# Kernel tuning notes

Measured on AMD Instinct MI355X. Metric: run time of the kernel, lower is better.

The kernel has to match this reference:

```python
import jax, jax.numpy as jnp
import numpy as np
import math

H = 16
D_MODEL = 1024
D_K = D_MODEL // H
B = 4
S = 2048


def setup_inputs() -> dict:
    key = jax.random.key(0)
    ks = jax.random.split(key, 11)
    s_in = 1.0 / math.sqrt(D_MODEL)
    inp = {
        "query": jax.random.normal(ks[0], (B, S, D_MODEL), dtype=jnp.float32),
        "key_": jax.random.normal(ks[1], (B, S, D_MODEL), dtype=jnp.float32),
        "value": jax.random.normal(ks[2], (B, S, D_MODEL), dtype=jnp.float32),
        # stacked per-head projection weights: [h, d_model, d_k]
        "Wq": jax.random.uniform(ks[3], (H, D_MODEL, D_K), jnp.float32, -s_in, s_in),
        "bq": jax.random.uniform(ks[4], (H, D_K), jnp.float32, -s_in, s_in),
        "Wk": jax.random.uniform(ks[5], (H, D_MODEL, D_K), jnp.float32, -s_in, s_in),
        "bk": jax.random.uniform(ks[6], (H, D_K), jnp.float32, -s_in, s_in),
        "Wv": jax.random.uniform(ks[7], (H, D_MODEL, D_K), jnp.float32, -s_in, s_in),
        "bv": jax.random.uniform(ks[8], (H, D_K), jnp.float32, -s_in, s_in),
        "Wo": jax.random.uniform(ks[9], (D_MODEL, D_MODEL), jnp.float32, -s_in, s_in),
        "bo": jax.random.uniform(ks[10], (D_MODEL,), jnp.float32, -s_in, s_in),
    }
    return inp


def reference(query, key_, value, Wq, bq, Wk, bk, Wv, bv, Wo, bo):
    # Per-head projections, batched over heads: [b,s,m] x [h,m,k] -> [b,h,s,k]
    q = jnp.einsum("bsm,hmk->bhsk", query, Wq) + bq[None, :, None, :]
    k = jnp.einsum("bsm,hmk->bhsk", key_, Wk) + bk[None, :, None, :]
    v = jnp.einsum("bsm,hmk->bhsk", value, Wv) + bv[None, :, None, :]
    # scores: q @ k^T -> [b,h,Sq,Sk]
    scores = jnp.einsum("bhqk,bhsk->bhqs", q, k) / jnp.sqrt(jnp.float32(D_K))
    # NOTE: original code softmaxes over dim=1 of the per-head [N,Sq,Sk]
    # tensor, i.e. the QUERY axis (axis=2 here). Mask has no effect
    # (masked_fill result is discarded in the source), so it is omitted.
    attn = jax.nn.softmax(scores, axis=2)
    ctx = jnp.einsum("bhqs,bhsk->bhqk", attn, v)  # [b,h,Sq,d_k]
    # concat heads along last dim (head-major order matches torch.cat)
    ctx = jnp.transpose(ctx, (0, 2, 1, 3)).reshape(B, S, D_MODEL)
    out = ctx @ Wo.T + bo  # final_W; dropout = identity (eval mode)
    return out
```

## Files before the change

### kernel.cpp

```cpp
#include <hip/hip_runtime.h>


#define DEV __device__ __forceinline__

typedef __bf16 bf16x8 __attribute__((ext_vector_type(8)));
typedef float  f32x4  __attribute__((ext_vector_type(4)));

DEV unsigned short f2bf(float f) {
    __bf16 h = (__bf16)f;
    return __builtin_bit_cast(unsigned short, h);
}

DEV bf16x8 ldfrag(const unsigned short* p) {
    return *reinterpret_cast<const bf16x8*>(p);
}

DEV float fast_exp2(float x) {
#if __has_builtin(__builtin_amdgcn_exp2f)
    return __builtin_amdgcn_exp2f(x);
#else
    return exp2f(x);
#endif
}

DEV void gld16(const unsigned short* g, unsigned short* l) {
    __builtin_amdgcn_global_load_lds(
        (__attribute__((address_space(1))) void*)g,
        (__attribute__((address_space(3))) void*)l, 16, 0, 0);
}

#define MFMA(a,b,c) __builtin_amdgcn_mfma_f32_16x16x32_bf16((a),(b),(c),0,0,0)

#define QSCALE 0.18033688011112042f

__global__ __launch_bounds__(256) void wprep(const float* __restrict__ Wq,
                                             const float* __restrict__ Wk,
                                             const float* __restrict__ Wv,
                                             const float* __restrict__ Wo,
                                             unsigned short* __restrict__ Wt,
                                             unsigned short* __restrict__ Wot) {
    int idx = blockIdx.x * 256 + threadIdx.x;
    int which = blockIdx.y;
    if (which == 3) { Wot[idx] = f2bf(Wo[idx]); return; }
    const float* W = (which == 0) ? Wq : (which == 1) ? Wk : Wv;
    int n = idx >> 10, m = idx & 1023;
    int h = n >> 6, k = n & 63;
    Wt[(size_t)which * 1048576 + idx] = f2bf(W[h * 65536 + m * 64 + k]);
}

__global__ __launch_bounds__(256) void xprep(const float* __restrict__ X,
                                             unsigned short* __restrict__ Xb) {
    int idx = (blockIdx.x * 256 + threadIdx.x) * 4;
    float4 f = *(const float4*)&X[idx];
    ushort4 o;
    o.x = f2bf(f.x); o.y = f2bf(f.y); o.z = f2bf(f.z); o.w = f2bf(f.w);
    *(ushort4*)&Xb[idx] = o;
}

__global__ __launch_bounds__(256) void proj_gemm(
        const unsigned short* __restrict__ Xb, const unsigned short* __restrict__ Bt,
        const float* __restrict__ bias, unsigned short* __restrict__ O,
        unsigned short* __restrict__ Vt, int z) {
    const int tid = threadIdx.x;
    const int bm = blockIdx.x, bn = blockIdx.y;

    __shared__ __align__(16) unsigned short As[128 * 32];
    __shared__ __align__(16) unsigned short Bs[128 * 32];

    const int lane = tid & 63, wid = tid >> 6;
    const int l16 = lane & 15, quad = lane >> 4;
    const int wm = wid & 1, wn = wid >> 1;

    const unsigned short* ga =
        Xb + (size_t)(bm * 128 + wid * 32 + (lane >> 2)) * 1024 + (lane & 3) * 8;
    const unsigned short* gb =
        Bt + (size_t)(bn * 128 + wid * 32 + (lane >> 2)) * 1024 + (lane & 3) * 8;
    unsigned short* la = &As[wid * 32 * 32];
    unsigned short* lb = &Bs[wid * 32 * 32];

    f32x4 acc[4][4] = {};
    for (int kt = 0; kt < 32; ++kt) {
        __syncthreads();
        const int k0 = kt * 32;
        gld16(ga + k0, la);
        gld16(ga + k0 + 16 * 1024, la + 16 * 32);
        gld16(gb + k0, lb);
        gld16(gb + k0 + 16 * 1024, lb + 16 * 32);
        __syncthreads();
        bf16x8 af[4], bfr[4];
#pragma unroll
        for (int mi = 0; mi < 4; ++mi)
            af[mi] = ldfrag(&As[(wm * 64 + mi * 16 + l16) * 32 + quad * 8]);
#pragma unroll
        for (int ni = 0; ni < 4; ++ni)
            bfr[ni] = ldfrag(&Bs[(wn * 64 + ni * 16 + l16) * 32 + quad * 8]);
#pragma unroll
        for (int mi = 0; mi < 4; ++mi)
#pragma unroll
            for (int ni = 0; ni < 4; ++ni)
                acc[mi][ni] = MFMA(af[mi], bfr[ni], acc[mi][ni]);
    }

#pragma unroll
    for (int mi = 0; mi < 4; ++mi)
#pragma unroll
        for (int ni = 0; ni < 4; ++ni)
#pragma unroll
            for (int r = 0; r < 4; ++r) {
                int row = bm * 128 + wm * 64 + mi * 16 + quad * 4 + r;
                int col = bn * 128 + wn * 64 + ni * 16 + l16;
                float v = acc[mi][ni][r] + bias[col];
                if (z == 0) v *= QSCALE;
                int b = row >> 11, s = row & 2047;
                int h = col >> 6, k = col & 63;
                unsigned short o = f2bf(v);
                if (z == 2) {
                    Vt[(size_t)((b * 16 + h) * 64 + k) * 2048 + s] = o;
                } else {
                    O[(size_t)((b * 16 + h) * 2048 + s) * 64 + k] = o;
                }
            }
}

__global__ __launch_bounds__(256) void colsum_vscale(
        const unsigned short* __restrict__ Qh, const unsigned short* __restrict__ Kh,
        unsigned short* __restrict__ Vt) {
    const int tid = threadIdx.x;
    const int st = blockIdx.x, bh = blockIdx.y;
    const unsigned short* Qb = Qh + (size_t)bh * 2048 * 64;
    const unsigned short* Kb = Kh + (size_t)bh * 2048 * 64;

    __shared__ __align__(16) unsigned short Qs[2][2][128 * 32];
    __shared__ float Dtmp[2][128];
    __shared__ float Dsh[128];

    const int lane = tid & 63, wid = tid >> 6;
    const int l16 = lane & 15, quad = lane >> 4;
    const int wm = wid & 1, wn = wid >> 1;

    bf16x8 kf[2][4];
#pragma unroll
    for (int ks = 0; ks < 2; ++ks)
#pragma unroll
        for (int ni = 0; ni < 4; ++ni)
            kf[ks][ni] = ldfrag(&Kb[(size_t)(st * 128 + wn * 64 + ni * 16 + l16) * 64 +
                                    ks * 32 + quad * 8]);

    const unsigned short* gq =
        Qb + (size_t)(wid * 32 + (lane >> 2)) * 64 + (lane & 3) * 8;

#pragma unroll
    for (int ks = 0; ks < 2; ++ks) {
        gld16(gq + ks * 32, &Qs[0][ks][wid * 32 * 32]);
        gld16(gq + (size_t)16 * 64 + ks * 32, &Qs[0][ks][(wid * 32 + 16) * 32]);
    }

    float psum[4] = {0.f, 0.f, 0.f, 0.f};
    for (int it = 0; it < 16; ++it) {
        const int buf = it & 1;
        __syncthreads();
        if (it < 15) {
            const size_t q1 = (size_t)(it + 1) * 128;
#pragma unroll
            for (int ks = 0; ks < 2; ++ks) {
                gld16(gq + q1 * 64 + ks * 32, &Qs[buf ^ 1][ks][wid * 32 * 32]);
                gld16(gq + (q1 + 16) * 64 + ks * 32,
                      &Qs[buf ^ 1][ks][(wid * 32 + 16) * 32]);
            }
        }
        f32x4 acc[4][4] = {};
#pragma unroll
        for (int ks = 0; ks < 2; ++ks) {
            bf16x8 af[4];
#pragma unroll
            for (int mi = 0; mi < 4; ++mi)
                af[mi] = ldfrag(&Qs[buf][ks][(wm * 64 + mi * 16 + l16) * 32 + quad * 8]);
#pragma unroll
            for (int mi = 0; mi < 4; ++mi)
#pragma unroll
                for (int ni = 0; ni < 4; ++ni)
                    acc[mi][ni] = MFMA(af[mi], kf[ks][ni], acc[mi][ni]);
        }
#pragma unroll
        for (int ni = 0; ni < 4; ++ni) {
            float d = 0.f;
#pragma unroll
            for (int mi = 0; mi < 4; ++mi)
#pragma unroll
                for (int r = 0; r < 4; ++r)
                    d += fast_exp2(acc[mi][ni][r]);
            psum[ni] += d;
        }
    }
#pragma unroll
    for (int ni = 0; ni < 4; ++ni) {
        float v = psum[ni];
        v += __shfl_xor(v, 16, 64);
        v += __shfl_xor(v, 32, 64);
        if (quad == 0) Dtmp[wm][wn * 64 + ni * 16 + l16] = v;
    }
    __syncthreads();
    if (tid < 128) Dsh[tid] = 1.0f / (Dtmp[0][tid] + Dtmp[1][tid]);
    __syncthreads();

    const int k = tid >> 2, c = tid & 3;
    unsigned short* vrow = Vt + ((size_t)bh * 64 + k) * 2048 + st * 128 + c * 32;
#pragma unroll
    for (int j = 0; j < 4; ++j) {
        bf16x8 v = *(const bf16x8*)&vrow[j * 8];
        bf16x8 o;
#pragma unroll
        for (int e = 0; e < 8; ++e)
            o[e] = (__bf16)((float)v[e] * Dsh[c * 32 + j * 8 + e]);
        *(bf16x8*)&vrow[j * 8] = o;
    }
}

__global__ __launch_bounds__(256) void attnpv(const unsigned short* __restrict__ Qh,
                                              const unsigned short* __restrict__ Kh,
                                              const unsigned short* __restrict__ Vn,
                                              unsigned short* __restrict__ Ctx) {
    const int tid = threadIdx.x;
    const int qt = blockIdx.x, bh = blockIdx.y;
    const int b = bh >> 4, h = bh & 15;
    const unsigned short* Qb = Qh + (size_t)bh * 2048 * 64;
    const unsigned short* Kb = Kh + (size_t)bh * 2048 * 64;
    const unsigned short* Vb = Vn + (size_t)bh * 64 * 2048;

    __shared__ __align__(16) unsigned short Ks[2][2][64 * 32];
    __shared__ __align__(16) unsigned short Vs[2][2][64 * 32];
    __shared__ __align__(16) unsigned short Ps[128 * 72];

    const int lane = tid & 63, wid = tid >> 6;
    const int l16 = lane & 15, quad = lane >> 4;
    const int wq = wid & 1, ws = wid >> 1;
    const int swz = (l16 & 3) << 3;

    bf16x8 qf[2][4];
#pragma unroll
    for (int ks = 0; ks < 2; ++ks)
#pragma unroll
        for (int nj = 0; nj < 4; ++nj)
            qf[ks][nj] = ldfrag(&Qb[(size_t)(qt * 128 + wq * 64 + nj * 16 + l16) * 64 +
                                    ks * 32 + quad * 8]);

    const int srow = lane >> 2, scol = (lane & 3) * 8, half = wid & 1;
    const unsigned short* gk = Kb + (size_t)srow * 64 + half * 32 + scol;
    const unsigned short* gv = Vb + (size_t)srow * 2048 + half * 32 + scol;

    if (wid < 2) {
#pragma unroll
        for (int gi = 0; gi < 4; ++gi)
            gld16(gk + (size_t)gi * 16 * 64, &Ks[0][half][gi * 16 * 32]);
    } else {
#pragma unroll
        for (int gi = 0; gi < 4; ++gi)
            gld16(gv + (size_t)gi * 16 * 2048, &Vs[0][half][gi * 16 * 32]);
    }

    f32x4 cacc[2][4] = {};
    for (int it = 0; it < 32; ++it) {
        const int buf = it & 1;
        const int s0 = it * 64;
        __syncthreads();

        bf16x8 kf[2][2];
#pragma unroll
        for (int mi = 0; mi < 2; ++mi)
#pragma unroll
            for (int ks = 0; ks < 2; ++ks)
                kf[mi][ks] = ldfrag(&Ks[buf][ks][(ws * 32 + mi * 16 + l16) * 32 + quad * 8]);
        f32x4 sacc[2][4] = {};
#pragma unroll
        for (int ks = 0; ks < 2; ++ks)
#pragma unroll
            for (int mi = 0; mi < 2; ++mi)
#pragma unroll
                for (int nj = 0; nj < 4; ++nj)
                    sacc[mi][nj] = MFMA(kf[mi][ks], qf[ks][nj], sacc[mi][nj]);

#pragma unroll
        for (int mi = 0; mi < 2; ++mi)
#pragma unroll
            for (int nj = 0; nj < 4; ++nj) {
                ushort4 p;
                p.x = f2bf(fast_exp2(sacc[mi][nj][0]));
                p.y = f2bf(fast_exp2(sacc[mi][nj][1]));
                p.z = f2bf(fast_exp2(sacc[mi][nj][2]));
                p.w = f2bf(fast_exp2(sacc[mi][nj][3]));
                *(ushort4*)&Ps[(size_t)(wq * 64 + nj * 16 + l16) * 72 +
                               ((ws * 32 + mi * 16 + quad * 4) ^ swz)] = p;
            }
        __syncthreads();

        if (it < 31) {
            if (wid < 2) {
#pragma unroll
                for (int gi = 0; gi < 4; ++gi)
                    gld16(gk + (size_t)(s0 + 64 + gi * 16) * 64,
                          &Ks[buf ^ 1][half][gi * 16 * 32]);
            } else {
#pragma unroll
                for (int gi = 0; gi < 4; ++gi)
                    gld16(gv + (size_t)(gi * 16) * 2048 + s0 + 64,
                          &Vs[buf ^ 1][half][gi * 16 * 32]);
            }
        }

        bf16x8 vf[2][2], pf[2][4];
#pragma unroll
        for (int mi = 0; mi < 2; ++mi)
#pragma unroll
            for (int ks2 = 0; ks2 < 2; ++ks2)
                vf[mi][ks2] = ldfrag(&Vs[buf][ks2][(ws * 32 + mi * 16 + l16) * 32 + quad * 8]);
#pragma unroll
        for (int ks2 = 0; ks2 < 2; ++ks2)
#pragma unroll
            for (int nj = 0; nj < 4; ++nj)
                pf[ks2][nj] = ldfrag(&Ps[(size_t)(wq * 64 + nj * 16 + l16) * 72 +
                                         ((ks2 * 32 + quad * 8) ^ swz)]);
#pragma unroll
        for (int ks2 = 0; ks2 < 2; ++ks2)
#pragma unroll
            for (int mi = 0; mi < 2; ++mi)
#pragma unroll
                for (int nj = 0; nj < 4; ++nj)
                    cacc[mi][nj] = MFMA(vf[mi][ks2], pf[ks2][nj], cacc[mi][nj]);
    }

#pragma unroll
    for (int mi = 0; mi < 2; ++mi)
#pragma unroll
        for (int nj = 0; nj < 4; ++nj) {
            int q = qt * 128 + wq * 64 + nj * 16 + l16;
            int k = ws * 32 + mi * 16 + quad * 4;
            ushort4 o;
            o.x = f2bf(cacc[mi][nj][0]);
            o.y = f2bf(cacc[mi][nj][1]);
            o.z = f2bf(cacc[mi][nj][2]);
            o.w = f2bf(cacc[mi][nj][3]);
            *(ushort4*)&Ctx[(size_t)(b * 2048 + q) * 1024 + h * 64 + k] = o;
        }
}

__global__ __launch_bounds__(256) void out_gemm(const unsigned short* __restrict__ A,
                                                const unsigned short* __restrict__ Bt,
                                                const float* __restrict__ bias,
                                                float* __restrict__ Out) {
    const int tid = threadIdx.x;
    const int bm = blockIdx.x, bn = blockIdx.y;

    __shared__ __align__(16) unsigned short As[128 * 32];
    __shared__ __align__(16) unsigned short Bs[128 * 32];

    const int lane = tid & 63, wid = tid >> 6;
    const int l16 = lane & 15, quad = lane >> 4;
    const int wm = wid & 1, wn = wid >> 1;

    const unsigned short* ga =
        A + (size_t)(bm * 128 + wid * 32 + (lane >> 2)) * 1024 + (lane & 3) * 8;
    const unsigned short* gb =
        Bt + (size_t)(bn * 128 + wid * 32 + (lane >> 2)) * 1024 + (lane & 3) * 8;
    unsigned short* la = &As[wid * 32 * 32];
    unsigned short* lb = &Bs[wid * 32 * 32];

    f32x4 acc[4][4] = {};
    for (int kt = 0; kt < 32; ++kt) {
        __syncthreads();
        const int k0 = kt * 32;
        gld16(ga + k0, la);
        gld16(ga + k0 + 16 * 1024, la + 16 * 32);
        gld16(gb + k0, lb);
        gld16(gb + k0 + 16 * 1024, lb + 16 * 32);
        __syncthreads();
        bf16x8 af[4], bfr[4];
#pragma unroll
        for (int mi = 0; mi < 4; ++mi)
            af[mi] = ldfrag(&As[(wm * 64 + mi * 16 + l16) * 32 + quad * 8]);
#pragma unroll
        for (int ni = 0; ni < 4; ++ni)
            bfr[ni] = ldfrag(&Bs[(wn * 64 + ni * 16 + l16) * 32 + quad * 8]);
#pragma unroll
        for (int mi = 0; mi < 4; ++mi)
#pragma unroll
            for (int ni = 0; ni < 4; ++ni)
                acc[mi][ni] = MFMA(af[mi], bfr[ni], acc[mi][ni]);
    }
#pragma unroll
    for (int mi = 0; mi < 4; ++mi)
#pragma unroll
        for (int ni = 0; ni < 4; ++ni)
#pragma unroll
            for (int r = 0; r < 4; ++r) {
                int row = bm * 128 + wm * 64 + mi * 16 + quad * 4 + r;
                int col = bn * 128 + wn * 64 + ni * 16 + l16;
                Out[(size_t)row * 1024 + col] = acc[mi][ni][r] + bias[col];
            }
}

extern "C" void kernel_launch(void* const* d_in, const int* in_sizes, int n_in,
                              void* d_out, int out_size, void* d_ws, size_t ws_size,
                              hipStream_t stream) {
    (void)in_sizes; (void)n_in; (void)out_size; (void)ws_size;
    const float* X[3] = {(const float*)d_in[0], (const float*)d_in[1],
                         (const float*)d_in[2]};
    const float* Wq = (const float*)d_in[3];
    const float* bq = (const float*)d_in[4];
    const float* Wk = (const float*)d_in[5];
    const float* bk = (const float*)d_in[6];
    const float* Wv = (const float*)d_in[7];
    const float* bv = (const float*)d_in[8];
    const float* Wo = (const float*)d_in[9];
    const float* bo = (const float*)d_in[10];
    const float* bias[3] = {bq, bk, bv};
    float* Out = (float*)d_out;

    char* ws = (char*)d_ws;
    const size_t MB = 1024 * 1024;
    unsigned short* Wt  = (unsigned short*)(ws);
    unsigned short* Wot = (unsigned short*)(ws + 6 * MB);
    unsigned short* Qh  = (unsigned short*)(ws + 8 * MB);
    unsigned short* Kh  = (unsigned short*)(ws + 24 * MB);
    unsigned short* Vt  = (unsigned short*)(ws + 40 * MB);
    unsigned short* Ctx = (unsigned short*)(ws + 56 * MB);
    unsigned short* Xb  = Ctx;
    unsigned short* Oz[3] = {Qh, Kh, Qh };

    wprep<<<dim3(4096, 4), dim3(256), 0, stream>>>(Wq, Wk, Wv, Wo, Wt, Wot);
    for (int z = 0; z < 3; ++z) {
        xprep<<<dim3(8192), dim3(256), 0, stream>>>(X[z], Xb);
        proj_gemm<<<dim3(64, 8), dim3(256), 0, stream>>>(
            Xb, Wt + (size_t)z * 1048576, bias[z], Oz[z], Vt, z);
    }
    colsum_vscale<<<dim3(16, 64), dim3(256), 0, stream>>>(Qh, Kh, Vt);
    attnpv<<<dim3(16, 64), dim3(256), 0, stream>>>(Qh, Kh, Vt, Ctx);
    out_gemm<<<dim3(64, 8), dim3(256), 0, stream>>>(Ctx, Wot, bo, Out);
}
```

Before: 456.6 us.

## Software-pipeline attention loop: overlap previous PV MFMA with current QK and exp

Restructures the attention main loop so the P·V product for the previous tile runs in the same iteration as the QK^T scores and exp of the current tile. The P buffer is double-buffered and V loads are moved to the start of each iteration. This drops one __syncthreads per iteration and lets exp/VALU work interleave with MFMA. In exchange, LDS use grows from about 34KB to about 52KB per block, which may lower occupancy, and an epilogue is added to finish the last PV step.

```diff
diff --git a/kernel.cpp b/kernel.cpp
--- a/kernel.cpp
+++ b/kernel.cpp
@@ -229,7 +229,7 @@
 
     __shared__ __align__(16) unsigned short Ks[2][2][64 * 32];
     __shared__ __align__(16) unsigned short Vs[2][2][64 * 32];
-    __shared__ __align__(16) unsigned short Ps[128 * 72];
+    __shared__ __align__(16) unsigned short Ps[2][128 * 72];
 
     const int lane = tid & 63, wid = tid >> 6;
     const int l16 = lane & 15, quad = lane >> 4;
@@ -252,24 +252,33 @@
 #pragma unroll
         for (int gi = 0; gi < 4; ++gi)
             gld16(gk + (size_t)gi * 16 * 64, &Ks[0][half][gi * 16 * 32]);
-    } else {
-#pragma unroll
-        for (int gi = 0; gi < 4; ++gi)
-            gld16(gv + (size_t)gi * 16 * 2048, &Vs[0][half][gi * 16 * 32]);
     }
 
     f32x4 cacc[2][4] = {};
     for (int it = 0; it < 32; ++it) {
-        const int buf = it & 1;
-        const int s0 = it * 64;
-        __syncthreads();
+        const int pb = it & 1;
+        __syncthreads();
+
+        if (wid < 2) {
+            if (it < 31) {
+                const size_t s1 = (size_t)(it + 1) * 64;
+#pragma unroll
+                for (int gi = 0; gi < 4; ++gi)
+                    gld16(gk + (s1 + gi * 16) * 64, &Ks[pb ^ 1][half][gi * 16 * 32]);
+            }
+        } else {
+#pragma unroll
+            for (int gi = 0; gi < 4; ++gi)
+                gld16(gv + (size_t)(gi * 16) * 2048 + it * 64,
+                      &Vs[pb][half][gi * 16 * 32]);
+        }
 
         bf16x8 kf[2][2];
 #pragma unroll
         for (int mi = 0; mi < 2; ++mi)
 #pragma unroll
             for (int ks = 0; ks < 2; ++ks)
-                kf[mi][ks] = ldfrag(&Ks[buf][ks][(ws * 32 + mi * 16 + l16) * 32 + quad * 8]);
+                kf[mi][ks] = ldfrag(&Ks[pb][ks][(ws * 32 + mi * 16 + l16) * 32 + quad * 8]);
         f32x4 sacc[2][4] = {};
 #pragma unroll
         for (int ks = 0; ks < 2; ++ks)
@@ -278,6 +287,22 @@
 #pragma unroll
                 for (int nj = 0; nj < 4; ++nj)
                     sacc[mi][nj] = MFMA(kf[mi][ks], qf[ks][nj], sacc[mi][nj]);
+
+        bf16x8 vf[2][2], pf2[2][4];
+        if (it > 0) {
+#pragma unroll
+            for (int mi = 0; mi < 2; ++mi)
+#pragma unroll
+                for (int ks2 = 0; ks2 < 2; ++ks2)
+                    vf[mi][ks2] =
+                        ldfrag(&Vs[pb ^ 1][ks2][(ws * 32 + mi * 16 + l16) * 32 + quad * 8]);
+#pragma unroll
+            for (int ks2 = 0; ks2 < 2; ++ks2)
+#pragma unroll
+                for (int nj = 0; nj < 4; ++nj)
+                    pf2[ks2][nj] = ldfrag(&Ps[pb ^ 1][(size_t)(wq * 64 + nj * 16 + l16) * 72 +
+                                              ((ks2 * 32 + quad * 8) ^ swz)]);
+        }
 
 #pragma unroll
         for (int mi = 0; mi < 2; ++mi)
@@ -288,44 +313,42 @@
                 p.y = f2bf(fast_exp2(sacc[mi][nj][1]));
                 p.z = f2bf(fast_exp2(sacc[mi][nj][2]));
                 p.w = f2bf(fast_exp2(sacc[mi][nj][3]));
-                *(ushort4*)&Ps[(size_t)(wq * 64 + nj * 16 + l16) * 72 +
-                               ((ws * 32 + mi * 16 + quad * 4) ^ swz)] = p;
+                *(ushort4*)&Ps[pb][(size_t)(wq * 64 + nj * 16 + l16) * 72 +
+                                   ((ws * 32 + mi * 16 + quad * 4) ^ swz)] = p;
             }
-        __syncthreads();
-
-        if (it < 31) {
-            if (wid < 2) {
-#pragma unroll
-                for (int gi = 0; gi < 4; ++gi)
-                    gld16(gk + (size_t)(s0 + 64 + gi * 16) * 64,
-                          &Ks[buf ^ 1][half][gi * 16 * 32]);
-            } else {
-#pragma unroll
-                for (int gi = 0; gi < 4; ++gi)
-                    gld16(gv + (size_t)(gi * 16) * 2048 + s0 + 64,
-                          &Vs[buf ^ 1][half][gi * 16 * 32]);
-            }
-        }
-
-        bf16x8 vf[2][2], pf[2][4];
+
+        if (it > 0) {
+#pragma unroll
+            for (int ks2 = 0; ks2 < 2; ++ks2)
+#pragma unroll
+                for (int mi = 0; mi < 2; ++mi)
+#pragma unroll
+                    for (int nj = 0; nj < 4; ++nj)
+                        cacc[mi][nj] = MFMA(vf[mi][ks2], pf2[ks2][nj], cacc[mi][nj]);
+        }
+    }
+
+    __syncthreads();
+    {
+        bf16x8 vf[2][2], pf2[2][4];
 #pragma unroll
         for (int mi = 0; mi < 2; ++mi)
 #pragma unroll
             for (int ks2 = 0; ks2 < 2; ++ks2)
-                vf[mi][ks2] = ldfrag(&Vs[buf][ks2][(ws * 32 + mi * 16 + l16) * 32 + quad * 8]);
+                vf[mi][ks2] = ldfrag(&Vs[1][ks2][(ws * 32 + mi * 16 + l16) * 32 + quad * 8]);
 #pragma unroll
         for (int ks2 = 0; ks2 < 2; ++ks2)
 #pragma unroll
             for (int nj = 0; nj < 4; ++nj)
-                pf[ks2][nj] = ldfrag(&Ps[(size_t)(wq * 64 + nj * 16 + l16) * 72 +
-                                         ((ks2 * 32 + quad * 8) ^ swz)]);
+                pf2[ks2][nj] = ldfrag(&Ps[1][(size_t)(wq * 64 + nj * 16 + l16) * 72 +
+                                          ((ks2 * 32 + quad * 8) ^ swz)]);
 #pragma unroll
         for (int ks2 = 0; ks2 < 2; ++ks2)
 #pragma unroll
             for (int mi = 0; mi < 2; ++mi)
 #pragma unroll
                 for (int nj = 0; nj < 4; ++nj)
-                    cacc[mi][nj] = MFMA(vf[mi][ks2], pf[ks2][nj], cacc[mi][nj]);
+                    cacc[mi][nj] = MFMA(vf[mi][ks2], pf2[ks2][nj], cacc[mi][nj]);
     }
 
 #pragma unroll
```

After: 454.1 us. About the same (-0.5%).

## Split PV over key halves per warp to drop mid-iteration block barrier

Applied to the files above, without the earlier changes.

Each warp now keeps its own private P tile in shared memory and does the PV product over only the key slice it computed, holding all 64 output columns. Because no warp reads another warp's P, the second __syncthreads per iteration goes away, and the K/V prefetch for the next tile is issued at the top of the loop. The cost is a doubled context accumulator (more registers) and a final cross-warp reduction through shared memory before the output is written.

```diff
diff --git a/kernel.cpp b/kernel.cpp
--- a/kernel.cpp
+++ b/kernel.cpp
@@ -227,14 +227,15 @@
     const unsigned short* Kb = Kh + (size_t)bh * 2048 * 64;
     const unsigned short* Vb = Vn + (size_t)bh * 64 * 2048;
 
-    __shared__ __align__(16) unsigned short Ks[2][2][64 * 32];
-    __shared__ __align__(16) unsigned short Vs[2][2][64 * 32];
-    __shared__ __align__(16) unsigned short Ps[128 * 72];
+    __shared__ __align__(16) unsigned char smem[49152];
+    unsigned short* Ks = (unsigned short*)smem;
+    unsigned short* Vs = (unsigned short*)(smem + 16384);
+    unsigned short* Pw = (unsigned short*)(smem + 32768) + (tid >> 6) * 2048;
 
     const int lane = tid & 63, wid = tid >> 6;
     const int l16 = lane & 15, quad = lane >> 4;
     const int wq = wid & 1, ws = wid >> 1;
-    const int swz = (l16 & 3) << 3;
+    const int pq = l16 & 3;
 
     bf16x8 qf[2][4];
 #pragma unroll
@@ -251,25 +252,40 @@
     if (wid < 2) {
 #pragma unroll
         for (int gi = 0; gi < 4; ++gi)
-            gld16(gk + (size_t)gi * 16 * 64, &Ks[0][half][gi * 16 * 32]);
+            gld16(gk + (size_t)gi * 16 * 64, &Ks[half * 2048 + gi * 16 * 32]);
     } else {
 #pragma unroll
         for (int gi = 0; gi < 4; ++gi)
-            gld16(gv + (size_t)gi * 16 * 2048, &Vs[0][half][gi * 16 * 32]);
-    }
-
-    f32x4 cacc[2][4] = {};
+            gld16(gv + (size_t)gi * 16 * 2048, &Vs[half * 2048 + gi * 16 * 32]);
+    }
+
+    f32x4 cacc[4][4] = {};
     for (int it = 0; it < 32; ++it) {
-        const int buf = it & 1;
-        const int s0 = it * 64;
-        __syncthreads();
+        const int pb = it & 1;
+        __syncthreads();
+
+        if (it < 31) {
+            const size_t s1 = (size_t)(it + 1) * 64;
+            if (wid < 2) {
+#pragma unroll
+                for (int gi = 0; gi < 4; ++gi)
+                    gld16(gk + (s1 + gi * 16) * 64,
+                          &Ks[((pb ^ 1) * 2 + half) * 2048 + gi * 16 * 32]);
+            } else {
+#pragma unroll
+                for (int gi = 0; gi < 4; ++gi)
+                    gld16(gv + (size_t)(gi * 16) * 2048 + s1,
+                          &Vs[((pb ^ 1) * 2 + half) * 2048 + gi * 16 * 32]);
+            }
+        }
 
         bf16x8 kf[2][2];
 #pragma unroll
         for (int mi = 0; mi < 2; ++mi)
 #pragma unroll
             for (int ks = 0; ks < 2; ++ks)
-                kf[mi][ks] = ldfrag(&Ks[buf][ks][(ws * 32 + mi * 16 + l16) * 32 + quad * 8]);
+                kf[mi][ks] = ldfrag(&Ks[(pb * 2 + ks) * 2048 +
+                                        (ws * 32 + mi * 16 + l16) * 32 + quad * 8]);
         f32x4 sacc[2][4] = {};
 #pragma unroll
         for (int ks = 0; ks < 2; ++ks)
@@ -280,7 +296,8 @@
                     sacc[mi][nj] = MFMA(kf[mi][ks], qf[ks][nj], sacc[mi][nj]);
 
 #pragma unroll
-        for (int mi = 0; mi < 2; ++mi)
+        for (int mi = 0; mi < 2; ++mi) {
+            const int gsw = ((mi * 2 + (quad >> 1)) ^ pq) * 8 + (quad & 1) * 4;
 #pragma unroll
             for (int nj = 0; nj < 4; ++nj) {
                 ushort4 p;
@@ -288,59 +305,50 @@
                 p.y = f2bf(fast_exp2(sacc[mi][nj][1]));
                 p.z = f2bf(fast_exp2(sacc[mi][nj][2]));
                 p.w = f2bf(fast_exp2(sacc[mi][nj][3]));
-                *(ushort4*)&Ps[(size_t)(wq * 64 + nj * 16 + l16) * 72 +
-                               ((ws * 32 + mi * 16 + quad * 4) ^ swz)] = p;
-            }
-        __syncthreads();
-
-        if (it < 31) {
-            if (wid < 2) {
-#pragma unroll
-                for (int gi = 0; gi < 4; ++gi)
-                    gld16(gk + (size_t)(s0 + 64 + gi * 16) * 64,
-                          &Ks[buf ^ 1][half][gi * 16 * 32]);
-            } else {
-#pragma unroll
-                for (int gi = 0; gi < 4; ++gi)
-                    gld16(gv + (size_t)(gi * 16) * 2048 + s0 + 64,
-                          &Vs[buf ^ 1][half][gi * 16 * 32]);
+                *(ushort4*)&Pw[(nj * 16 + l16) * 32 + gsw] = p;
             }
         }
 
-        bf16x8 vf[2][2], pf[2][4];
-#pragma unroll
-        for (int mi = 0; mi < 2; ++mi)
-#pragma unroll
-            for (int ks2 = 0; ks2 < 2; ++ks2)
-                vf[mi][ks2] = ldfrag(&Vs[buf][ks2][(ws * 32 + mi * 16 + l16) * 32 + quad * 8]);
-#pragma unroll
-        for (int ks2 = 0; ks2 < 2; ++ks2)
+        bf16x8 vf[4], pf[4];
+#pragma unroll
+        for (int mi = 0; mi < 4; ++mi)
+            vf[mi] = ldfrag(&Vs[(pb * 2 + ws) * 2048 + (mi * 16 + l16) * 32 + quad * 8]);
+#pragma unroll
+        for (int nj = 0; nj < 4; ++nj)
+            pf[nj] = ldfrag(&Pw[(nj * 16 + l16) * 32 + (quad ^ pq) * 8]);
+#pragma unroll
+        for (int mi = 0; mi < 4; ++mi)
 #pragma unroll
             for (int nj = 0; nj < 4; ++nj)
-                pf[ks2][nj] = ldfrag(&Ps[(size_t)(wq * 64 + nj * 16 + l16) * 72 +
-                                         ((ks2 * 32 + quad * 8) ^ swz)]);
-#pragma unroll
-        for (int ks2 = 0; ks2 < 2; ++ks2)
-#pragma unroll
-            for (int mi = 0; mi < 2; ++mi)
-#pragma unroll
-                for (int nj = 0; nj < 4; ++nj)
-                    cacc[mi][nj] = MFMA(vf[mi][ks2], pf[ks2][nj], cacc[mi][nj]);
-    }
-
-#pragma unroll
-    for (int mi = 0; mi < 2; ++mi)
-#pragma unroll
-        for (int nj = 0; nj < 4; ++nj) {
-            int q = qt * 128 + wq * 64 + nj * 16 + l16;
-            int k = ws * 32 + mi * 16 + quad * 4;
-            ushort4 o;
-            o.x = f2bf(cacc[mi][nj][0]);
-            o.y = f2bf(cacc[mi][nj][1]);
-            o.z = f2bf(cacc[mi][nj][2]);
-            o.w = f2bf(cacc[mi][nj][3]);
-            *(ushort4*)&Ctx[(size_t)(b * 2048 + q) * 1024 + h * 64 + k] = o;
-        }
+                cacc[mi][nj] = MFMA(vf[mi], pf[nj], cacc[mi][nj]);
+    }
+
+    __syncthreads();
+    f32x4* Red = (f32x4*)smem;
+    if (ws == 1) {
+#pragma unroll
+        for (int mi = 0; mi < 4; ++mi)
+#pragma unroll
+            for (int nj = 0; nj < 4; ++nj)
+                Red[(wq * 16 + mi * 4 + nj) * 64 + lane] = cacc[mi][nj];
+    }
+    __syncthreads();
+    if (ws == 0) {
+#pragma unroll
+        for (int mi = 0; mi < 4; ++mi)
+#pragma unroll
+            for (int nj = 0; nj < 4; ++nj) {
+                f32x4 t = Red[(wq * 16 + mi * 4 + nj) * 64 + lane];
+                int q = qt * 128 + wq * 64 + nj * 16 + l16;
+                int k = mi * 16 + quad * 4;
+                ushort4 o;
+                o.x = f2bf(cacc[mi][nj][0] + t[0]);
+                o.y = f2bf(cacc[mi][nj][1] + t[1]);
+                o.z = f2bf(cacc[mi][nj][2] + t[2]);
+                o.w = f2bf(cacc[mi][nj][3] + t[3]);
+                *(ushort4*)&Ctx[(size_t)(b * 2048 + q) * 1024 + h * 64 + k] = o;
+            }
+    }
 }
 
 __global__ __launch_bounds__(256) void out_gemm(const unsigned short* __restrict__ A,
```

Result: faster. 440.8 us (-3.4%).
